# Optimization experiments

Measured on AMD Instinct MI355X. Metric: run time of the kernel, lower is better.

## Reference

```python
import math
import jax, jax.numpy as jnp
import numpy as np

B, S, D = 1, 2048, 4096
H, KV, Dh = 32, 8, 128          # query heads, kv heads, head dim
G = H // KV                      # GQA group size
THETA = 10000.0
FACTOR = 4.0
BETA_FAST, BETA_SLOW, ORIG_MAX = 32, 1, 32768


def _yarn_rope_cache(seq_len):
    """YaRN-scaled RoPE cos/sin cache, matching YaRNRotaryEmbedding._build_cache."""
    inv_freq = 1.0 / (THETA ** (np.arange(0, Dh, 2, dtype=np.float32) / Dh))
    low = ORIG_MAX / (2 * math.pi * BETA_SLOW)
    high = ORIG_MAX / (2 * math.pi * BETA_FAST)
    freq = 1.0 / inv_freq
    smooth = np.clip((freq - low) / (high - low), 0.0, 1.0)
    inv_freq = (1.0 - smooth) * inv_freq + smooth * (inv_freq / FACTOR)
    t = np.arange(seq_len, dtype=np.float32)
    freqs = np.outer(t, inv_freq)                 # [S, Dh/2]
    emb = np.concatenate([freqs, freqs], axis=-1) # [S, Dh]
    return np.cos(emb).astype(np.float32), np.sin(emb).astype(np.float32)


def _rotate_half(x):
    x1, x2 = jnp.split(x, 2, axis=-1)
    return jnp.concatenate([-x2, x1], axis=-1)


def setup_inputs() -> dict:
    key = jax.random.key(0)
    k0, k1, k2, k3, k4 = jax.random.split(key, 5)
    scale = 0.02
    hidden_states = jax.random.normal(k0, (B, S, D), jnp.float32)
    Wq = jax.random.normal(k1, (H * Dh, D), jnp.float32) * scale
    Wk = jax.random.normal(k2, (KV * Dh, D), jnp.float32) * scale
    Wv = jax.random.normal(k3, (KV * Dh, D), jnp.float32) * scale
    Wo = jax.random.normal(k4, (D, H * Dh), jnp.float32) * scale
    cos_np, sin_np = _yarn_rope_cache(S)
    return {"hidden_states": hidden_states, "Wq": Wq, "Wk": Wk, "Wv": Wv,
            "Wo": Wo, "cos": jnp.asarray(cos_np), "sin": jnp.asarray(sin_np)}


def reference(hidden_states, Wq, Wk, Wv, Wo, cos, sin):
    x = hidden_states
    b, s, _ = x.shape
    # QKV projections (Linear, no bias): y = x @ W.T
    q = jnp.einsum('bsd,ed->bse', x, Wq).reshape(b, s, H, Dh).transpose(0, 2, 1, 3)   # [B,H,S,Dh]
    k = jnp.einsum('bsd,ed->bse', x, Wk).reshape(b, s, KV, Dh).transpose(0, 2, 1, 3)  # [B,KV,S,Dh]
    v = jnp.einsum('bsd,ed->bse', x, Wv).reshape(b, s, KV, Dh).transpose(0, 2, 1, 3)  # [B,KV,S,Dh]
    # YaRN RoPE (cos/sin: [S,Dh], broadcast over batch/head)
    c = cos[None, None, :, :]
    sn = sin[None, None, :, :]
    q = q * c + _rotate_half(q) * sn
    k = k * c + _rotate_half(k) * sn
    # GQA: group query heads over kv heads instead of materializing repeat_interleave
    qg = q.reshape(b, KV, G, s, Dh)
    scores = jnp.einsum('bkgqd,bknd->bkgqn', qg, k) / math.sqrt(Dh)  # [B,KV,G,S,S]
    causal = jnp.tril(jnp.ones((s, s), dtype=bool))
    scores = jnp.where(causal[None, None, None], scores, jnp.finfo(scores.dtype).min)
    w = jax.nn.softmax(scores.astype(jnp.float32), axis=-1).astype(x.dtype)
    attn = jnp.einsum('bkgqn,bknd->bkgqd', w, v)                      # [B,KV,G,S,Dh]
    attn = attn.reshape(b, H, s, Dh).transpose(0, 2, 1, 3).reshape(b, s, H * Dh)
    return jnp.einsum('bse,de->bsd', attn, Wo)
```

## Files before the change

### kernel.cpp

```cpp
#include <hip/hip_runtime.h>

#define S_LEN 2048
#define DMODEL 4096
#define NH 32
#define NKV 8
#define DH 128
#define QDIM (NH*DH)
#define NQKV 6144
#define SCALE 0.08838834764831845f

typedef __attribute__((ext_vector_type(8))) short short8;
typedef __attribute__((ext_vector_type(4))) float f32x4;
typedef __attribute__((ext_vector_type(4))) unsigned short us4;

__device__ __forceinline__ unsigned short f2bf(float f) {
  union { float f; unsigned int u; } v; v.f = f;
  unsigned int r = v.u + 0x7FFFu + ((v.u >> 16) & 1u);
  return (unsigned short)(r >> 16);
}
__device__ __forceinline__ float bf2f(unsigned short h) {
  union { unsigned int u; float f; } v; v.u = ((unsigned int)h) << 16;
  return v.f;
}

__global__ __launch_bounds__(256) void cvt_all(const float* __restrict__ x,
                                               const float* __restrict__ Wq,
                                               const float* __restrict__ Wk,
                                               const float* __restrict__ Wv,
                                               const float* __restrict__ Wo,
                                               unsigned short* __restrict__ xb,
                                               unsigned short* __restrict__ Wqkvb,
                                               unsigned short* __restrict__ Wob) {
  const int blk = blockIdx.x;
  const float* src; unsigned short* dst; int off;
  if (blk < 8192)       { src = x;  dst = xb;               off = blk; }
  else if (blk < 24576) { src = Wq; dst = Wqkvb;            off = blk - 8192; }
  else if (blk < 28672) { src = Wk; dst = Wqkvb + 16777216; off = blk - 24576; }
  else if (blk < 32768) { src = Wv; dst = Wqkvb + 20971520; off = blk - 28672; }
  else                  { src = Wo; dst = Wob;              off = blk - 32768; }
  int i = off * 256 + threadIdx.x;
  const float4 f = reinterpret_cast<const float4*>(src)[i];
  us4 o;
  o.x = f2bf(f.x); o.y = f2bf(f.y); o.z = f2bf(f.z); o.w = f2bf(f.w);
  reinterpret_cast<us4*>(dst)[i] = o;
}

template<int M_, int N_, int K_, int BM_, int BN_, int OUT_BF16, int CHN>
__global__ __launch_bounds__(512) void gemm8p(const unsigned short* __restrict__ A,
                                              const unsigned short* __restrict__ B,
                                              void* __restrict__ Cv) {
  constexpr int ATILE = BM_ * 128;
  constexpr int BTILE = BN_ * 128;
  constexpr int BUF = ATILE + BTILE;
  constexpr int LPA = BM_ / 64;
  constexpr int LPB = BN_ / 64;
  constexpr int VM  = LPA + LPB;
  constexpr int MI = BM_ / 32, NF = BN_ / 64;
  constexpr int MIL = MI / 2, NFL = NF / 2;
  constexpr int NT = K_ / 64;
  __shared__ char lds[2 * BUF];

  const int tid = threadIdx.x;
  const int lane = tid & 63, wave = tid >> 6;
  const int wm = wave >> 2, wn = wave & 3;
  const int fr = lane & 15, fq = lane >> 4;

  const int lin = blockIdx.x;
  const int xcd = lin & 7;
  const int slot = lin >> 3;
  const long n0 = (long)(xcd * CHN + slot % CHN) * BN_;
  const long m0 = (long)(slot / CHN) * BM_;

  auto STAGE_A = [&](int t, int c) {
#pragma unroll
    for (int u = 0; u < LPA; ++u) {
      int b = u * 8192 + tid * 16;
      int row = b >> 7;
      int off = (b & 127) ^ ((row & 7) << 4);
      __builtin_amdgcn_global_load_lds(
        (const __attribute__((address_space(1))) void*)((const char*)A + ((m0 + row) * (long)K_ + t * 64) * 2 + off),
        (__attribute__((address_space(3))) void*)(lds + c * BUF + b), 16, 0, 0);
    }
  };
  auto STAGE_B = [&](int t, int c) {
#pragma unroll
    for (int u = 0; u < LPB; ++u) {
      int b = u * 8192 + tid * 16;
      int row = b >> 7;
      int off = (b & 127) ^ ((row & 7) << 4);
      __builtin_amdgcn_global_load_lds(
        (const __attribute__((address_space(1))) void*)((const char*)B + ((n0 + row) * (long)K_ + t * 64) * 2 + off),
        (__attribute__((address_space(3))) void*)(lds + c * BUF + ATILE + b), 16, 0, 0);
    }
  };
#define VMCNT_STEADY() do { if constexpr (VM == 6) asm volatile("s_waitcnt vmcnt(6)" ::: "memory"); \
                            else if constexpr (VM == 7) asm volatile("s_waitcnt vmcnt(7)" ::: "memory"); \
                            else asm volatile("s_waitcnt vmcnt(8)" ::: "memory"); } while (0)

  f32x4 acc[MI][NF] = {};
  short8 af[MI][2];
  short8 bf[NF][2];

  STAGE_A(0, 0); STAGE_B(0, 0);
  STAGE_A(1, 1); STAGE_B(1, 1);
  VMCNT_STEADY();
  __builtin_amdgcn_s_barrier();

  for (int t = 0; t < NT; ++t) {
    const int c = t & 1;
    const char* tb = lds + c * BUF;

#pragma unroll
    for (int mi = 0; mi < MIL; ++mi) {
      int row = wm * (BM_ / 2) + mi * 16 + fr;
#pragma unroll
      for (int ks = 0; ks < 2; ++ks)
        af[mi][ks] = *(const short8*)(tb + row * 128 + ((ks * 64 + fq * 16) ^ ((row & 7) << 4)));
    }
#pragma unroll
    for (int ni = 0; ni < NFL; ++ni) {
      int row = wn * (BN_ / 4) + ni * 16 + fr;
#pragma unroll
      for (int ks = 0; ks < 2; ++ks)
        bf[ni][ks] = *(const short8*)(tb + ATILE + row * 128 + ((ks * 64 + fq * 16) ^ ((row & 7) << 4)));
    }
    __builtin_amdgcn_s_barrier();
    __builtin_amdgcn_s_setprio(1);
#pragma unroll
    for (int mi = 0; mi < MIL; ++mi)
#pragma unroll
      for (int ni = 0; ni < NFL; ++ni)
#pragma unroll
        for (int ks = 0; ks < 2; ++ks)
          acc[mi][ni] = __builtin_amdgcn_mfma_f32_16x16x32_bf16(af[mi][ks], bf[ni][ks], acc[mi][ni], 0, 0, 0);
    __builtin_amdgcn_s_setprio(0);
    __builtin_amdgcn_s_barrier();

#pragma unroll
    for (int mi = MIL; mi < MI; ++mi) {
      int row = wm * (BM_ / 2) + mi * 16 + fr;
#pragma unroll
      for (int ks = 0; ks < 2; ++ks)
        af[mi][ks] = *(const short8*)(tb + row * 128 + ((ks * 64 + fq * 16) ^ ((row & 7) << 4)));
    }
#pragma unroll
    for (int ni = NFL; ni < NF; ++ni) {
      int row = wn * (BN_ / 4) + ni * 16 + fr;
#pragma unroll
      for (int ks = 0; ks < 2; ++ks)
        bf[ni][ks] = *(const short8*)(tb + ATILE + row * 128 + ((ks * 64 + fq * 16) ^ ((row & 7) << 4)));
    }
    __builtin_amdgcn_s_barrier();
    __builtin_amdgcn_s_setprio(1);
#pragma unroll
    for (int mi = 0; mi < MIL; ++mi)
#pragma unroll
      for (int ni = NFL; ni < NF; ++ni)
#pragma unroll
        for (int ks = 0; ks < 2; ++ks)
          acc[mi][ni] = __builtin_amdgcn_mfma_f32_16x16x32_bf16(af[mi][ks], bf[ni][ks], acc[mi][ni], 0, 0, 0);
    __builtin_amdgcn_s_setprio(0);
    __builtin_amdgcn_s_barrier();

    if (t + 2 < NT) STAGE_A(t + 2, c);
    __builtin_amdgcn_s_setprio(1);
#pragma unroll
    for (int mi = MIL; mi < MI; ++mi)
#pragma unroll
      for (int ni = 0; ni < NFL; ++ni)
#pragma unroll
        for (int ks = 0; ks < 2; ++ks)
          acc[mi][ni] = __builtin_amdgcn_mfma_f32_16x16x32_bf16(af[mi][ks], bf[ni][ks], acc[mi][ni], 0, 0, 0);
    __builtin_amdgcn_s_setprio(0);
    __builtin_amdgcn_s_barrier();

    if (t + 2 < NT) STAGE_B(t + 2, c);
    __builtin_amdgcn_s_setprio(1);
#pragma unroll
    for (int mi = MIL; mi < MI; ++mi)
#pragma unroll
      for (int ni = NFL; ni < NF; ++ni)
#pragma unroll
        for (int ks = 0; ks < 2; ++ks)
          acc[mi][ni] = __builtin_amdgcn_mfma_f32_16x16x32_bf16(af[mi][ks], bf[ni][ks], acc[mi][ni], 0, 0, 0);
    __builtin_amdgcn_s_setprio(0);
    if (t + 2 < NT) { VMCNT_STEADY(); }
    else if (t + 1 < NT) { asm volatile("s_waitcnt vmcnt(0)" ::: "memory"); }
    __builtin_amdgcn_s_barrier();
  }
#undef VMCNT_STEADY

#pragma unroll
  for (int mi = 0; mi < MI; ++mi)
#pragma unroll
    for (int ni = 0; ni < NF; ++ni)
#pragma unroll
      for (int j = 0; j < 4; ++j) {
        long r = m0 + wm * (BM_ / 2) + mi * 16 + fq * 4 + j;
        long cc = n0 + wn * (BN_ / 4) + ni * 16 + fr;
        float v = acc[mi][ni][j];
        if (OUT_BF16) ((unsigned short*)Cv)[r * N_ + cc] = f2bf(v);
        else          ((float*)Cv)[r * N_ + cc] = v;
      }
}

template<int M_, int N_, int K_, int BM_, int BN_, int OUT_BF16, int CHN>
__global__ __launch_bounds__(512) void gemm8p3(const unsigned short* __restrict__ A,
                                               const unsigned short* __restrict__ B,
                                               void* __restrict__ Cv) {
  constexpr int ATILE = BM_ * 128;
  constexpr int BTILE = BN_ * 128;
  constexpr int BUF = ATILE + BTILE;
  constexpr int LPA = BM_ / 64;
  constexpr int LPB = BN_ / 64;
  constexpr int VM  = LPA + LPB;
  constexpr int MI = BM_ / 32, NF = BN_ / 64;
  constexpr int MIL = MI / 2, NFL = NF / 2;
  constexpr int NT = K_ / 64;
  __shared__ char lds[3 * BUF];

  const int tid = threadIdx.x;
  const int lane = tid & 63, wave = tid >> 6;
  const int wm = wave >> 2, wn = wave & 3;
  const int fr = lane & 15, fq = lane >> 4;

  const int lin = blockIdx.x;
  const int xcd = lin & 7;
  const int slot = lin >> 3;
  const long n0 = (long)(xcd * CHN + slot % CHN) * BN_;
  const long m0 = (long)(slot / CHN) * BM_;

  auto STAGE_A = [&](int t, int c) {
#pragma unroll
    for (int u = 0; u < LPA; ++u) {
      int b = u * 8192 + tid * 16;
      int row = b >> 7;
      int off = (b & 127) ^ ((row & 7) << 4);
      __builtin_amdgcn_global_load_lds(
        (const __attribute__((address_space(1))) void*)((const char*)A + ((m0 + row) * (long)K_ + t * 64) * 2 + off),
        (__attribute__((address_space(3))) void*)(lds + c * BUF + b), 16, 0, 0);
    }
  };
  auto STAGE_B_HALF = [&](int t, int c, int half) {
#pragma unroll
    for (int u = 0; u < LPB / 2; ++u) {
      int b = (half * (LPB / 2) + u) * 8192 + tid * 16;
      int row = b >> 7;
      int off = (b & 127) ^ ((row & 7) << 4);
      __builtin_amdgcn_global_load_lds(
        (const __attribute__((address_space(1))) void*)((const char*)B + ((n0 + row) * (long)K_ + t * 64) * 2 + off),
        (__attribute__((address_space(3))) void*)(lds + c * BUF + ATILE + b), 16, 0, 0);
    }
  };

  f32x4 acc[MI][NF] = {};
  short8 af[MI][2];
  short8 bf[NF][2];

  STAGE_A(0, 0); STAGE_B_HALF(0, 0, 0); STAGE_B_HALF(0, 0, 1);
  STAGE_A(1, 1); STAGE_B_HALF(1, 1, 0); STAGE_B_HALF(1, 1, 1);
  asm volatile("s_waitcnt vmcnt(0)" ::: "memory");
  __builtin_amdgcn_s_barrier();

  for (int t = 0; t < NT; ++t) {
    const char* tb = lds + (t % 3) * BUF;
    const int c2 = (t + 2) % 3;

#pragma unroll
    for (int mi = 0; mi < MIL; ++mi) {
      int row = wm * (BM_ / 2) + mi * 16 + fr;
#pragma unroll
      for (int ks = 0; ks < 2; ++ks)
        af[mi][ks] = *(const short8*)(tb + row * 128 + ((ks * 64 + fq * 16) ^ ((row & 7) << 4)));
    }
#pragma unroll
    for (int ni = 0; ni < NFL; ++ni) {
      int row = wn * (BN_ / 4) + ni * 16 + fr;
#pragma unroll
      for (int ks = 0; ks < 2; ++ks)
        bf[ni][ks] = *(const short8*)(tb + ATILE + row * 128 + ((ks * 64 + fq * 16) ^ ((row & 7) << 4)));
    }
    if (t + 2 < NT) STAGE_A(t + 2, c2);
    __builtin_amdgcn_s_barrier();
    __builtin_amdgcn_s_setprio(1);
#pragma unroll
    for (int mi = 0; mi < MIL; ++mi)
#pragma unroll
      for (int ni = 0; ni < NFL; ++ni)
#pragma unroll
        for (int ks = 0; ks < 2; ++ks)
          acc[mi][ni] = __builtin_amdgcn_mfma_f32_16x16x32_bf16(af[mi][ks], bf[ni][ks], acc[mi][ni], 0, 0, 0);
    __builtin_amdgcn_s_setprio(0);
    __builtin_amdgcn_s_barrier();

#pragma unroll
    for (int mi = MIL; mi < MI; ++mi) {
      int row = wm * (BM_ / 2) + mi * 16 + fr;
#pragma unroll
      for (int ks = 0; ks < 2; ++ks)
        af[mi][ks] = *(const short8*)(tb + row * 128 + ((ks * 64 + fq * 16) ^ ((row & 7) << 4)));
    }
#pragma unroll
    for (int ni = NFL; ni < NF; ++ni) {
      int row = wn * (BN_ / 4) + ni * 16 + fr;
#pragma unroll
      for (int ks = 0; ks < 2; ++ks)
        bf[ni][ks] = *(const short8*)(tb + ATILE + row * 128 + ((ks * 64 + fq * 16) ^ ((row & 7) << 4)));
    }
    if (t + 2 < NT) STAGE_B_HALF(t + 2, c2, 0);
    __builtin_amdgcn_s_barrier();
    __builtin_amdgcn_s_setprio(1);
#pragma unroll
    for (int mi = 0; mi < MIL; ++mi)
#pragma unroll
      for (int ni = NFL; ni < NF; ++ni)
#pragma unroll
        for (int ks = 0; ks < 2; ++ks)
          acc[mi][ni] = __builtin_amdgcn_mfma_f32_16x16x32_bf16(af[mi][ks], bf[ni][ks], acc[mi][ni], 0, 0, 0);
    __builtin_amdgcn_s_setprio(0);
    __builtin_amdgcn_s_barrier();

    if (t + 2 < NT) STAGE_B_HALF(t + 2, c2, 1);
    __builtin_amdgcn_s_setprio(1);
#pragma unroll
    for (int mi = MIL; mi < MI; ++mi)
#pragma unroll
      for (int ni = 0; ni < NFL; ++ni)
#pragma unroll
        for (int ks = 0; ks < 2; ++ks)
          acc[mi][ni] = __builtin_amdgcn_mfma_f32_16x16x32_bf16(af[mi][ks], bf[ni][ks], acc[mi][ni], 0, 0, 0);
    __builtin_amdgcn_s_setprio(0);
    __builtin_amdgcn_s_barrier();

    __builtin_amdgcn_s_setprio(1);
#pragma unroll
    for (int mi = MIL; mi < MI; ++mi)
#pragma unroll
      for (int ni = NFL; ni < NF; ++ni)
#pragma unroll
        for (int ks = 0; ks < 2; ++ks)
          acc[mi][ni] = __builtin_amdgcn_mfma_f32_16x16x32_bf16(af[mi][ks], bf[ni][ks], acc[mi][ni], 0, 0, 0);
    __builtin_amdgcn_s_setprio(0);
    if (t + 2 < NT) { asm volatile("s_waitcnt vmcnt(6)" ::: "memory"); }
    else if (t + 1 < NT) { asm volatile("s_waitcnt vmcnt(0)" ::: "memory"); }
    __builtin_amdgcn_s_barrier();
  }
  (void)VM;

#pragma unroll
  for (int mi = 0; mi < MI; ++mi)
#pragma unroll
    for (int ni = 0; ni < NF; ++ni)
#pragma unroll
      for (int j = 0; j < 4; ++j) {
        long r = m0 + wm * (BM_ / 2) + mi * 16 + fq * 4 + j;
        long cc = n0 + wn * (BN_ / 4) + ni * 16 + fr;
        float v = acc[mi][ni][j];
        if (OUT_BF16) ((unsigned short*)Cv)[r * N_ + cc] = f2bf(v);
        else          ((float*)Cv)[r * N_ + cc] = v;
      }
}

__global__ __launch_bounds__(256) void rope_fused(unsigned short* __restrict__ C,
                                                  const float* __restrict__ cosb,
                                                  const float* __restrict__ sinb) {
  int idx = blockIdx.x * 256 + threadIdx.x;
  int i = idx & 63;
  int t = idx >> 6;
  int hh = t % 40;
  int s = t / 40;
  const bool isQ = hh < 32;
  unsigned short* row = C + (size_t)s * NQKV + (isQ ? hh * DH : 4096 + (hh - 32) * DH);
  float sc = isQ ? SCALE : 1.0f;
  float c  = cosb[s * DH + i];
  float sn = sinb[s * DH + i];
  float x1 = bf2f(row[i]);
  float x2 = bf2f(row[i + 64]);
  row[i]      = f2bf((x1 * c - x2 * sn) * sc);
  row[i + 64] = f2bf((x2 * c + x1 * sn) * sc);
}

__global__ __launch_bounds__(256) void transpose_v(const unsigned short* __restrict__ Vbuf,
                                                   unsigned short* __restrict__ VT) {
  __shared__ unsigned short t[64][72];
  const int s0 = blockIdx.x * 64, e0 = blockIdx.y * 64;
  const int r = threadIdx.x >> 3, c = (threadIdx.x & 7) * 8;
#pragma unroll
  for (int half = 0; half < 2; ++half) {
    int row = r + half * 32;
    *reinterpret_cast<short8*>(&t[row][c]) =
        *reinterpret_cast<const short8*>(Vbuf + (size_t)(s0 + row) * NQKV + e0 + c);
  }
  __syncthreads();
  const int hh = e0 >> 7, dbase = e0 & 127;
#pragma unroll
  for (int half = 0; half < 2; ++half) {
    int row = r + half * 32;
    short8 o;
#pragma unroll
    for (int j = 0; j < 8; ++j) ((unsigned short*)&o)[j] = t[c + j][row];
    *reinterpret_cast<short8*>(VT + (size_t)hh * (DH * (size_t)S_LEN)
                               + (size_t)(dbase + row) * S_LEN + s0 + c) = o;
  }
}

__global__ __launch_bounds__(256) void attn_fwd(const unsigned short* __restrict__ C,
                                                const unsigned short* __restrict__ VT,
                                                unsigned short* __restrict__ Ob) {
  __shared__ unsigned short KVs[2][8192];
  __shared__ unsigned short Pl[4][16 * 40];
  const int tid = threadIdx.x, lane = tid & 63, wave = tid >> 6;
  const int kvh = blockIdx.x & 7;
  const int p = blockIdx.x >> 3;
  const int h = kvh * 4 + wave;
  const int fr = lane & 15, fq = lane >> 4;
  const int q0s[2] = { p * 16, (127 - p) * 16 };
  const int tilesA = (p * 16 + 47) >> 5;
  const int tilesB = ((127 - p) * 16 + 47) >> 5;

  const unsigned short* Qbase = C + (size_t)h * DH;
  const unsigned short* Kbase = C + 4096 + (size_t)kvh * DH;
  const unsigned short* Vbase = VT + (size_t)kvh * (DH * (size_t)S_LEN);

  short8 qf[2][4];
#pragma unroll
  for (int s = 0; s < 2; ++s)
#pragma unroll
    for (int dc = 0; dc < 4; ++dc)
      qf[s][dc] = *reinterpret_cast<const short8*>(
          Qbase + (size_t)(q0s[s] + fr) * NQKV + dc * 32 + fq * 8);

  f32x4 o_acc[2][8] = {};
  float mrow[2][4] = {{-1e30f,-1e30f,-1e30f,-1e30f},{-1e30f,-1e30f,-1e30f,-1e30f}};
  float lpart[2][4] = {};

  auto STAGE = [&](int t, int buf) {
    const int kv0 = t * 32;
    char* dst = (char*)&KVs[buf][0];
#pragma unroll
    for (int sh = 0; sh < 2; ++sh) {
      int b = sh * 4096 + tid * 16;
      int krow = b >> 8;
      int kcol = (b & 255) ^ ((krow & 7) << 4);
      __builtin_amdgcn_global_load_lds(
          (const __attribute__((address_space(1))) void*)(Kbase + (size_t)(kv0 + krow) * NQKV + (kcol >> 1)),
          (__attribute__((address_space(3))) void*)(dst + b), 16, 0, 0);
      int vrow = b >> 6;
      int vcol = (b & 63) ^ ((((vrow ^ (vrow >> 2)) & 3)) << 4);
      __builtin_amdgcn_global_load_lds(
          (const __attribute__((address_space(1))) void*)(Vbase + (size_t)vrow * S_LEN + kv0 + (vcol >> 1)),
          (__attribute__((address_space(3))) void*)(dst + 8192 + b), 16, 0, 0);
    }
  };

  int cur = 0;
  STAGE(0, 0);
  asm volatile("s_waitcnt vmcnt(0)" ::: "memory");
  __syncthreads();

  for (int t = 0; t < tilesB; ++t) {
    const int kv0 = t * 32;
    if (t + 1 < tilesB) STAGE(t + 1, cur ^ 1);
    const char* kvb = (const char*)&KVs[cur][0];

#pragma unroll
    for (int s = 0; s < 2; ++s) {
      if (s == 0 && t >= tilesA) continue;
      const int q0 = q0s[s];

      f32x4 sacc[2] = {};
#pragma unroll
      for (int nt = 0; nt < 2; ++nt) {
        const int row = nt * 16 + fr;
#pragma unroll
        for (int dc = 0; dc < 4; ++dc) {
          short8 kf = *reinterpret_cast<const short8*>(
              kvb + row * 256 + ((dc * 64 + fq * 16) ^ ((row & 7) << 4)));
          sacc[nt] = __builtin_amdgcn_mfma_f32_16x16x32_bf16(qf[s][dc], kf, sacc[nt], 0, 0, 0);
        }
      }

      const bool needMask = (kv0 + 32 > q0);
      if (needMask) {
#pragma unroll
        for (int j = 0; j < 4; ++j) {
          int qrow = q0 + fq * 4 + j;
#pragma unroll
          for (int nt = 0; nt < 2; ++nt)
            sacc[nt][j] = ((kv0 + nt*16 + fr) <= qrow) ? sacc[nt][j] : -1e30f;
        }
      }
      bool ok = true;
      float lm[4];
#pragma unroll
      for (int j = 0; j < 4; ++j) {
        lm[j] = fmaxf(sacc[0][j], sacc[1][j]);
        ok = ok && (lm[j] <= mrow[s][j] + 8.f);
      }
      if (!__all(ok)) {
#pragma unroll
        for (int j = 0; j < 4; ++j) {
          float rm = lm[j];
          rm = fmaxf(rm, __shfl_xor(rm, 1));
          rm = fmaxf(rm, __shfl_xor(rm, 2));
          rm = fmaxf(rm, __shfl_xor(rm, 4));
          rm = fmaxf(rm, __shfl_xor(rm, 8));
          float mnew = fmaxf(mrow[s][j], rm);
          float corr = __expf(mrow[s][j] - mnew);
          mrow[s][j] = mnew;
          lpart[s][j] *= corr;
#pragma unroll
          for (int dt = 0; dt < 8; ++dt) o_acc[s][dt][j] *= corr;
        }
      }
#pragma unroll
      for (int j = 0; j < 4; ++j) {
        float p0 = __expf(sacc[0][j] - mrow[s][j]);
        float p1 = __expf(sacc[1][j] - mrow[s][j]);
        lpart[s][j] += p0 + p1;
        unsigned int u;
        asm("v_cvt_pk_bf16_f32 %0, %1, %2" : "=v"(u) : "v"(p0), "v"(p1));
        Pl[wave][(fq*4 + j)*40 + fr]      = (unsigned short)u;
        Pl[wave][(fq*4 + j)*40 + 16 + fr] = (unsigned short)(u >> 16);
      }
      asm volatile("s_waitcnt lgkmcnt(0)" ::: "memory");
      __builtin_amdgcn_sched_barrier(0);

      short8 pa = *reinterpret_cast<const short8*>(&Pl[wave][fr*40 + fq*8]);
#pragma unroll
      for (int dt = 0; dt < 8; ++dt) {
        const int row = dt * 16 + fr;
        short8 bv = *reinterpret_cast<const short8*>(
            kvb + 8192 + row * 64 + ((fq * 16) ^ ((((row ^ (row >> 2)) & 3)) << 4)));
        o_acc[s][dt] = __builtin_amdgcn_mfma_f32_16x16x32_bf16(pa, bv, o_acc[s][dt], 0, 0, 0);
      }
    }

    asm volatile("s_waitcnt vmcnt(0)" ::: "memory");
    __syncthreads();
    cur ^= 1;
  }

#pragma unroll
  for (int s = 0; s < 2; ++s)
#pragma unroll
    for (int j = 0; j < 4; ++j) {
      float l = lpart[s][j];
      l += __shfl_xor(l, 1);
      l += __shfl_xor(l, 2);
      l += __shfl_xor(l, 4);
      l += __shfl_xor(l, 8);
      float inv = 1.f / l;
      size_t r = (size_t)q0s[s] + fq*4 + j;
#pragma unroll
      for (int dt = 0; dt < 8; ++dt)
        Ob[r * QDIM + h * DH + dt*16 + fr] = f2bf(o_acc[s][dt][j] * inv);
    }
}

extern "C" void kernel_launch(void* const* d_in, const int* in_sizes, int n_in,
                              void* d_out, int out_size, void* d_ws, size_t ws_size,
                              hipStream_t stream) {
  (void)in_sizes; (void)n_in; (void)out_size; (void)ws_size;
  const float* x    = (const float*)d_in[0];
  const float* Wq   = (const float*)d_in[1];
  const float* Wk   = (const float*)d_in[2];
  const float* Wv   = (const float*)d_in[3];
  const float* Wo   = (const float*)d_in[4];
  const float* cosb = (const float*)d_in[5];
  const float* sinb = (const float*)d_in[6];

  char* ws = (char*)d_ws;
  unsigned short* xb    = (unsigned short*)(ws);
  unsigned short* Wqkvb = (unsigned short*)(ws + 16777216);
  unsigned short* Wob   = (unsigned short*)(ws + 67108864);
  unsigned short* Cqkv  = (unsigned short*)(ws + 100663296);
  unsigned short* VT    = (unsigned short*)(ws + 125829120);
  unsigned short* Ab    = xb;

  cvt_all<<<49152, 256, 0, stream>>>(x, Wq, Wk, Wv, Wo, xb, Wqkvb, Wob);

  gemm8p<2048, 6144, 4096, 256, 192, 1, 4><<<256, 512, 0, stream>>>(xb, Wqkvb, Cqkv);

  rope_fused<<<20480, 256, 0, stream>>>(Cqkv, cosb, sinb);
  transpose_v<<<dim3(32, 16), 256, 0, stream>>>(Cqkv + 5120, VT);

  attn_fwd<<<512, 256, 0, stream>>>(Cqkv, VT, Ab);

  gemm8p3<2048, 4096, 4096, 128, 256, 0, 2><<<256, 512, 0, stream>>>(Ab, Wob, d_out);
}
```

Measured before the change: 306.0 us.

## Fuse RoPE into QKV GEMM epilogue via interleaved weight row permutation

After: 311.7 us. No clear change (+1.9%).

```diff
diff --git a/kernel.cpp b/kernel.cpp
--- a/kernel.cpp
+++ b/kernel.cpp
@@ -32,37 +32,47 @@
                                                unsigned short* __restrict__ Wqkvb,
                                                unsigned short* __restrict__ Wob) {
   const int blk = blockIdx.x;
-  const float* src; unsigned short* dst; int off;
+  const float* src; unsigned short* dst; int off; int perm = 0;
   if (blk < 8192)       { src = x;  dst = xb;               off = blk; }
-  else if (blk < 24576) { src = Wq; dst = Wqkvb;            off = blk - 8192; }
-  else if (blk < 28672) { src = Wk; dst = Wqkvb + 16777216; off = blk - 24576; }
+  else if (blk < 24576) { src = Wq; dst = Wqkvb;            off = blk - 8192; perm = 1; }
+  else if (blk < 28672) { src = Wk; dst = Wqkvb + 16777216; off = blk - 24576; perm = 1; }
   else if (blk < 32768) { src = Wv; dst = Wqkvb + 20971520; off = blk - 28672; }
   else                  { src = Wo; dst = Wob;              off = blk - 32768; }
   int i = off * 256 + threadIdx.x;
-  const float4 f = reinterpret_cast<const float4*>(src)[i];
+  int si = i;
+  if (perm) {
+    int n = i >> 10, q = i & 1023;
+    int m = n & 127;
+    int srcrow = (n & ~127) | ((m & 1) ? ((m >> 1) + 64) : (m >> 1));
+    si = srcrow * 1024 + q;
+  }
+  const float4 f = reinterpret_cast<const float4*>(src)[si];
   us4 o;
   o.x = f2bf(f.x); o.y = f2bf(f.y); o.z = f2bf(f.z); o.w = f2bf(f.w);
   reinterpret_cast<us4*>(dst)[i] = o;
 }
 
-template<int M_, int N_, int K_, int BM_, int BN_, int OUT_BF16, int CHN>
+template<int M_, int N_, int K_, int BM_, int BN_, int WM_, int OUT_BF16, int CHN, int ROPE_>
 __global__ __launch_bounds__(512) void gemm8p(const unsigned short* __restrict__ A,
                                               const unsigned short* __restrict__ B,
-                                              void* __restrict__ Cv) {
+                                              void* __restrict__ Cv,
+                                              const float* __restrict__ cosb,
+                                              const float* __restrict__ sinb) {
+  constexpr int WN_ = 8 / WM_;
   constexpr int ATILE = BM_ * 128;
   constexpr int BTILE = BN_ * 128;
   constexpr int BUF = ATILE + BTILE;
   constexpr int LPA = BM_ / 64;
   constexpr int LPB = BN_ / 64;
   constexpr int VM  = LPA + LPB;
-  constexpr int MI = BM_ / 32, NF = BN_ / 64;
+  constexpr int MI = BM_ / (16 * WM_), NF = BN_ / (16 * WN_);
   constexpr int MIL = MI / 2, NFL = NF / 2;
   constexpr int NT = K_ / 64;
   __shared__ char lds[2 * BUF];
 
   const int tid = threadIdx.x;
   const int lane = tid & 63, wave = tid >> 6;
-  const int wm = wave >> 2, wn = wave & 3;
+  const int wm = wave / WN_, wn = wave % WN_;
   const int fr = lane & 15, fq = lane >> 4;
 
   const int lin = blockIdx.x;
@@ -112,14 +122,14 @@
 
 #pragma unroll
     for (int mi = 0; mi < MIL; ++mi) {
-      int row = wm * (BM_ / 2) + mi * 16 + fr;
+      int row = wm * (BM_ / WM_) + mi * 16 + fr;
 #pragma unroll
       for (int ks = 0; ks < 2; ++ks)
         af[mi][ks] = *(const short8*)(tb + row * 128 + ((ks * 64 + fq * 16) ^ ((row & 7) << 4)));
     }
 #pragma unroll
     for (int ni = 0; ni < NFL; ++ni) {
-      int row = wn * (BN_ / 4) + ni * 16 + fr;
+      int row = wn * (BN_ / WN_) + ni * 16 + fr;
 #pragma unroll
       for (int ks = 0; ks < 2; ++ks)
         bf[ni][ks] = *(const short8*)(tb + ATILE + row * 128 + ((ks * 64 + fq * 16) ^ ((row & 7) << 4)));
@@ -138,14 +148,14 @@
 
 #pragma unroll
     for (int mi = MIL; mi < MI; ++mi) {
-      int row = wm * (BM_ / 2) + mi * 16 + fr;
+      int row = wm * (BM_ / WM_) + mi * 16 + fr;
 #pragma unroll
       for (int ks = 0; ks < 2; ++ks)
         af[mi][ks] = *(const short8*)(tb + row * 128 + ((ks * 64 + fq * 16) ^ ((row & 7) << 4)));
     }
 #pragma unroll
     for (int ni = NFL; ni < NF; ++ni) {
-      int row = wn * (BN_ / 4) + ni * 16 + fr;
+      int row = wn * (BN_ / WN_) + ni * 16 + fr;
 #pragma unroll
       for (int ks = 0; ks < 2; ++ks)
         bf[ni][ks] = *(const short8*)(tb + ATILE + row * 128 + ((ks * 64 + fq * 16) ^ ((row & 7) << 4)));
@@ -196,9 +206,21 @@
     for (int ni = 0; ni < NF; ++ni)
 #pragma unroll
       for (int j = 0; j < 4; ++j) {
-        long r = m0 + wm * (BM_ / 2) + mi * 16 + fq * 4 + j;
-        long cc = n0 + wn * (BN_ / 4) + ni * 16 + fr;
+        long r = m0 + wm * (BM_ / WM_) + mi * 16 + fq * 4 + j;
+        long cc = n0 + wn * (BN_ / WN_) + ni * 16 + fr;
         float v = acc[mi][ni][j];
+        if constexpr (ROPE_) {
+          float w = __shfl_xor(v, 1);
+          if (cc < 5120) {
+            int i = ((int)cc & 127) >> 1;
+            float cs = cosb[r * 128 + i];
+            float sn = sinb[r * 128 + i];
+            float x1 = (fr & 1) ? w : v;
+            float x2 = (fr & 1) ? v : w;
+            v = (fr & 1) ? (x2 * cs + x1 * sn) : (x1 * cs - x2 * sn);
+            if (cc < 4096) v *= SCALE;
+          }
+        } else { (void)cosb; (void)sinb; }
         if (OUT_BF16) ((unsigned short*)Cv)[r * N_ + cc] = f2bf(v);
         else          ((float*)Cv)[r * N_ + cc] = v;
       }
@@ -213,7 +235,6 @@
   constexpr int BUF = ATILE + BTILE;
   constexpr int LPA = BM_ / 64;
   constexpr int LPB = BN_ / 64;
-  constexpr int VM  = LPA + LPB;
   constexpr int MI = BM_ / 32, NF = BN_ / 64;
   constexpr int MIL = MI / 2, NFL = NF / 2;
   constexpr int NT = K_ / 64;
@@ -345,7 +366,6 @@
     else if (t + 1 < NT) { asm volatile("s_waitcnt vmcnt(0)" ::: "memory"); }
     __builtin_amdgcn_s_barrier();
   }
-  (void)VM;
 
 #pragma unroll
   for (int mi = 0; mi < MI; ++mi)
@@ -359,25 +379,6 @@
         if (OUT_BF16) ((unsigned short*)Cv)[r * N_ + cc] = f2bf(v);
         else          ((float*)Cv)[r * N_ + cc] = v;
       }
-}
-
-__global__ __launch_bounds__(256) void rope_fused(unsigned short* __restrict__ C,
-                                                  const float* __restrict__ cosb,
-                                                  const float* __restrict__ sinb) {
-  int idx = blockIdx.x * 256 + threadIdx.x;
-  int i = idx & 63;
-  int t = idx >> 6;
-  int hh = t % 40;
-  int s = t / 40;
-  const bool isQ = hh < 32;
-  unsigned short* row = C + (size_t)s * NQKV + (isQ ? hh * DH : 4096 + (hh - 32) * DH);
-  float sc = isQ ? SCALE : 1.0f;
-  float c  = cosb[s * DH + i];
-  float sn = sinb[s * DH + i];
-  float x1 = bf2f(row[i]);
-  float x2 = bf2f(row[i + 64]);
-  row[i]      = f2bf((x1 * c - x2 * sn) * sc);
-  row[i + 64] = f2bf((x2 * c + x1 * sn) * sc);
 }
 
 __global__ __launch_bounds__(256) void transpose_v(const unsigned short* __restrict__ Vbuf,
@@ -580,9 +581,9 @@
 
   cvt_all<<<49152, 256, 0, stream>>>(x, Wq, Wk, Wv, Wo, xb, Wqkvb, Wob);
 
-  gemm8p<2048, 6144, 4096, 256, 192, 1, 4><<<256, 512, 0, stream>>>(xb, Wqkvb, Cqkv);
-
-  rope_fused<<<20480, 256, 0, stream>>>(Cqkv, cosb, sinb);
+  gemm8p<2048, 6144, 4096, 256, 192, 4, 1, 4, 1>
+      <<<256, 512, 0, stream>>>(xb, Wqkvb, Cqkv, cosb, sinb);
+
   transpose_v<<<dim3(32, 16), 256, 0, stream>>>(Cqkv + 5120, VT);
 
   attn_fwd<<<512, 256, 0, stream>>>(Cqkv, VT, Ab);
```
